# Kernel tuning notes

Measured on AMD Instinct MI355X. Metric: run time of the kernel, lower is better.

## Reference

```python
import jax, jax.numpy as jnp
import numpy as np

N_EXPERTS = 8
D_MODEL = 1024
D_FF = 4096


def setup_inputs() -> dict:
    key = jax.random.key(0)
    k_x, k_idx, k_g, k_u, k_d = jax.random.split(key, 5)
    scale_in = 1.0 / np.sqrt(D_MODEL)
    scale_ff = 1.0 / np.sqrt(D_FF)
    return {
        "x": jax.random.normal(k_x, (2, 1024, D_MODEL), dtype=jnp.float32),
        "expert_idx": jax.random.randint(k_idx, (2, 1024), 0, N_EXPERTS, dtype=jnp.int64),
        "w_gate": jax.random.normal(k_g, (N_EXPERTS, D_MODEL, D_FF), dtype=jnp.float32) * scale_in,
        "w_up": jax.random.normal(k_u, (N_EXPERTS, D_MODEL, D_FF), dtype=jnp.float32) * scale_in,
        "w_down": jax.random.normal(k_d, (N_EXPERTS, D_FF, D_MODEL), dtype=jnp.float32) * scale_ff,
    }


def reference(x, expert_idx, w_gate, w_up, w_down):
    # x: [B, S, D]; expert_idx: [B, S] in [0, N_EXPERTS)
    B, S, D = x.shape
    x_flat = x.reshape(-1, D)                  # [T, D]
    idx_flat = expert_idx.reshape(-1)          # [T]
    out = jnp.zeros_like(x_flat)
    # Faithful per-expert dispatch: each token is processed by exactly one
    # expert's SwiGLU FFN; masked scatter-back combines results.
    for e in range(N_EXPERTS):
        mask = (idx_flat == e)[:, None]        # [T, 1]
        gate = jax.nn.silu(x_flat @ w_gate[e]) # [T, F]
        up = x_flat @ w_up[e]                  # [T, F]
        y = (gate * up) @ w_down[e]            # [T, D]
        out = jnp.where(mask, y, out)
    return out.reshape(B, S, D)
```

## Files before the change

kernel.cpp:

```cpp
#include <hip/hip_runtime.h>
#include <hip/hip_bf16.h>
#include <stdint.h>

#define N_EXPERTS 8
#define D_MODEL   1024
#define D_FF      4096
#define T_TOKENS  2048
#define MT        128
#define MAXT      24
#define KPAD      40

typedef __attribute__((ext_vector_type(8))) short bf16x8;
typedef __attribute__((ext_vector_type(4))) float f32x4;

__device__ __forceinline__ short f2bf(float f) {
    union { float f; uint32_t u; } v; v.f = f;
    uint32_t u = v.u;
    uint32_t r = (u + 0x7fffu + ((u >> 16) & 1u)) >> 16;
    return (short)r;
}

__device__ __forceinline__ uint32_t pack2bf(float a, float b) {
    __hip_bfloat162 h = __float22bfloat162_rn(make_float2(a, b));
    return *(uint32_t*)&h;
}


__global__ void moe_count(const int* __restrict__ idx, int* __restrict__ counts) {
    int t = blockIdx.x * blockDim.x + threadIdx.x;
    if (t < T_TOKENS) atomicAdd(&counts[idx[t]], 1);
}

__global__ void moe_scan(const int* __restrict__ counts, int* __restrict__ offsets,
                         int* __restrict__ ntiles, int* __restrict__ tile_e,
                         int* __restrict__ tile_p0, int* __restrict__ tile_end) {
    if (threadIdx.x == 0 && blockIdx.x == 0) {
        int off = 0, nt = 0;
        for (int e = 0; e < N_EXPERTS; ++e) {
            offsets[e] = off;
            int c = counts[e];
            int end = off + c;
            for (int i = 0; i < c; i += MT) {
                tile_e[nt] = e;
                tile_p0[nt] = off + i;
                tile_end[nt] = end;
                ++nt;
            }
            off = end;
        }
        offsets[N_EXPERTS] = off;
        *ntiles = nt;
    }
}

__global__ void moe_gather(const float* __restrict__ x, const int* __restrict__ idx,
                           const int* __restrict__ offsets, int* __restrict__ cursor,
                           int* __restrict__ tok_of_row, short* __restrict__ Xg) {
    __shared__ int sp;
    int t = blockIdx.x;
    if (threadIdx.x == 0) {
        int e = idx[t];
        int p = offsets[e] + atomicAdd(&cursor[e], 1);
        tok_of_row[p] = t;
        sp = p;
    }
    __syncthreads();
    int p = sp;
    const float4* src = (const float4*)(x + (size_t)t * D_MODEL);
    uint2* dst = (uint2*)(Xg + (size_t)p * D_MODEL);
    int i = threadIdx.x;
    float4 v = src[i];
    uint2 o;
    o.x = pack2bf(v.x, v.y);
    o.y = pack2bf(v.z, v.w);
    dst[i] = o;
}


__launch_bounds__(256)
__global__ void moe_gemm1(const float* __restrict__ wg, const float* __restrict__ wu,
                          const short* __restrict__ Xg, short* __restrict__ h,
                          const int* __restrict__ tile_e, const int* __restrict__ tile_p0,
                          const int* __restrict__ tile_end, const int* __restrict__ ntiles) {
    int ti = blockIdx.y;
    if (ti >= *ntiles) return;
    int e = tile_e[ti], p0 = tile_p0[ti], pend = tile_end[ti];
    int n0 = blockIdx.x * 64;

    __shared__ short Bg[64][KPAD];
    __shared__ short Bu[64][KPAD];

    int tid = threadIdx.x;
    int nl = tid & 63, kc = tid >> 6;
    int lane = tid & 63, w = tid >> 6;
    int col = lane & 15, quad = lane >> 4;

    const float* wgb = wg + (size_t)e * D_MODEL * D_FF + n0 + nl;
    const float* wub = wu + (size_t)e * D_MODEL * D_FF + n0 + nl;

    int row0 = p0 + w * 32 + col;      if (row0 > T_TOKENS - 1) row0 = T_TOKENS - 1;
    int row1 = row0 + 16;              if (row1 > T_TOKENS - 1) row1 = T_TOKENS - 1;
    const short* a0p = Xg + (size_t)row0 * D_MODEL + quad * 8;
    const short* a1p = Xg + (size_t)row1 * D_MODEL + quad * 8;

    f32x4 accg[2][4], accu[2][4];
#pragma unroll
    for (int m = 0; m < 2; ++m)
#pragma unroll
        for (int nf = 0; nf < 4; ++nf) {
            accg[m][nf] = (f32x4){0,0,0,0};
            accu[m][nf] = (f32x4){0,0,0,0};
        }

    for (int k0 = 0; k0 < D_MODEL; k0 += 32) {
        {
            const float* g = wgb + (size_t)(k0 + kc * 8) * D_FF;
            const float* u = wub + (size_t)(k0 + kc * 8) * D_FF;
            float gv[8], uv[8];
#pragma unroll
            for (int j = 0; j < 8; ++j) {
                gv[j] = g[(size_t)j * D_FF];
                uv[j] = u[(size_t)j * D_FF];
            }
            uint4 pg, pu;
            pg.x = pack2bf(gv[0], gv[1]); pg.y = pack2bf(gv[2], gv[3]);
            pg.z = pack2bf(gv[4], gv[5]); pg.w = pack2bf(gv[6], gv[7]);
            pu.x = pack2bf(uv[0], uv[1]); pu.y = pack2bf(uv[2], uv[3]);
            pu.z = pack2bf(uv[4], uv[5]); pu.w = pack2bf(uv[6], uv[7]);
            *(uint4*)&Bg[nl][kc * 8] = pg;
            *(uint4*)&Bu[nl][kc * 8] = pu;
        }
        __syncthreads();
        bf16x8 a0 = *(const bf16x8*)(a0p + k0);
        bf16x8 a1 = *(const bf16x8*)(a1p + k0);
#pragma unroll
        for (int nf = 0; nf < 4; ++nf) {
            bf16x8 bg = *(const bf16x8*)&Bg[nf * 16 + col][quad * 8];
            bf16x8 bu = *(const bf16x8*)&Bu[nf * 16 + col][quad * 8];
            accg[0][nf] = __builtin_amdgcn_mfma_f32_16x16x32_bf16(a0, bg, accg[0][nf], 0, 0, 0);
            accg[1][nf] = __builtin_amdgcn_mfma_f32_16x16x32_bf16(a1, bg, accg[1][nf], 0, 0, 0);
            accu[0][nf] = __builtin_amdgcn_mfma_f32_16x16x32_bf16(a0, bu, accu[0][nf], 0, 0, 0);
            accu[1][nf] = __builtin_amdgcn_mfma_f32_16x16x32_bf16(a1, bu, accu[1][nf], 0, 0, 0);
        }
        __syncthreads();
    }

#pragma unroll
    for (int m = 0; m < 2; ++m) {
#pragma unroll
        for (int r = 0; r < 4; ++r) {
            int mr = p0 + w * 32 + m * 16 + quad * 4 + r;
            if (mr < pend) {
#pragma unroll
                for (int nf = 0; nf < 4; ++nf) {
                    float gv = accg[m][nf][r], uv = accu[m][nf][r];
                    float hv = (gv / (1.f + __expf(-gv))) * uv;
                    h[(size_t)mr * D_FF + n0 + nf * 16 + col] = f2bf(hv);
                }
            }
        }
    }
}


__launch_bounds__(256)
__global__ void moe_gemm2(const float* __restrict__ wd, const short* __restrict__ h,
                          const int* __restrict__ tok_of_row, float* __restrict__ out,
                          const int* __restrict__ tile_e, const int* __restrict__ tile_p0,
                          const int* __restrict__ tile_end, const int* __restrict__ ntiles) {
    int ti = blockIdx.y;
    if (ti >= *ntiles) return;
    int e = tile_e[ti], p0 = tile_p0[ti], pend = tile_end[ti];
    int d0 = blockIdx.x * 64;

    __shared__ short Bd[64][KPAD];

    int tid = threadIdx.x;
    int nl = tid & 63, kc = tid >> 6;
    int lane = tid & 63, w = tid >> 6;
    int col = lane & 15, quad = lane >> 4;

    const float* wb = wd + (size_t)e * D_FF * D_MODEL + d0 + nl;

    int row0 = p0 + w * 32 + col;      if (row0 > T_TOKENS - 1) row0 = T_TOKENS - 1;
    int row1 = row0 + 16;              if (row1 > T_TOKENS - 1) row1 = T_TOKENS - 1;
    const short* a0p = h + (size_t)row0 * D_FF + quad * 8;
    const short* a1p = h + (size_t)row1 * D_FF + quad * 8;

    f32x4 acc[2][4];
#pragma unroll
    for (int m = 0; m < 2; ++m)
#pragma unroll
        for (int nf = 0; nf < 4; ++nf) acc[m][nf] = (f32x4){0,0,0,0};

    for (int k0 = 0; k0 < D_FF; k0 += 32) {
        {
            const float* p = wb + (size_t)(k0 + kc * 8) * D_MODEL;
            float pv[8];
#pragma unroll
            for (int j = 0; j < 8; ++j) pv[j] = p[(size_t)j * D_MODEL];
            uint4 pk;
            pk.x = pack2bf(pv[0], pv[1]); pk.y = pack2bf(pv[2], pv[3]);
            pk.z = pack2bf(pv[4], pv[5]); pk.w = pack2bf(pv[6], pv[7]);
            *(uint4*)&Bd[nl][kc * 8] = pk;
        }
        __syncthreads();
        bf16x8 a0 = *(const bf16x8*)(a0p + k0);
        bf16x8 a1 = *(const bf16x8*)(a1p + k0);
#pragma unroll
        for (int nf = 0; nf < 4; ++nf) {
            bf16x8 b = *(const bf16x8*)&Bd[nf * 16 + col][quad * 8];
            acc[0][nf] = __builtin_amdgcn_mfma_f32_16x16x32_bf16(a0, b, acc[0][nf], 0, 0, 0);
            acc[1][nf] = __builtin_amdgcn_mfma_f32_16x16x32_bf16(a1, b, acc[1][nf], 0, 0, 0);
        }
        __syncthreads();
    }

#pragma unroll
    for (int m = 0; m < 2; ++m) {
#pragma unroll
        for (int r = 0; r < 4; ++r) {
            int mr = p0 + w * 32 + m * 16 + quad * 4 + r;
            if (mr < pend) {
                int t = tok_of_row[mr];
#pragma unroll
                for (int nf = 0; nf < 4; ++nf)
                    out[(size_t)t * D_MODEL + d0 + nf * 16 + col] = acc[m][nf][r];
            }
        }
    }
}


extern "C" void kernel_launch(void* const* d_in, const int* in_sizes, int n_in,
                              void* d_out, int out_size, void* d_ws, size_t ws_size,
                              hipStream_t stream) {
    (void)in_sizes; (void)n_in; (void)out_size; (void)ws_size;
    const float* x   = (const float*)d_in[0];
    const int*   idx = (const int*)d_in[1];
    const float* wg  = (const float*)d_in[2];
    const float* wu  = (const float*)d_in[3];
    const float* wd  = (const float*)d_in[4];
    float* out = (float*)d_out;

    int* ws_i       = (int*)d_ws;
    int* counts     = ws_i;
    int* cursor     = ws_i + 8;
    int* offsets    = ws_i + 16;
    int* ntiles     = ws_i + 25;
    int* tile_e     = ws_i + 32;
    int* tile_p0    = ws_i + 104;
    int* tile_end   = ws_i + 176;
    int* tok_of_row = ws_i + 256;

    short* Xg = (short*)((char*)d_ws + 16384);
    short* h  = (short*)((char*)d_ws + 16384 + (size_t)T_TOKENS * D_MODEL * 2);

    hipMemsetAsync(d_ws, 0, 1024, stream);
    moe_count<<<dim3((T_TOKENS + 255) / 256), 256, 0, stream>>>(idx, counts);
    moe_scan<<<dim3(1), 64, 0, stream>>>(counts, offsets, ntiles, tile_e, tile_p0, tile_end);
    moe_gather<<<dim3(T_TOKENS), 256, 0, stream>>>(x, idx, offsets, cursor, tok_of_row, Xg);
    moe_gemm1<<<dim3(D_FF / 64, MAXT), 256, 0, stream>>>(wg, wu, Xg, h,
                                                         tile_e, tile_p0, tile_end, ntiles);
    moe_gemm2<<<dim3(D_MODEL / 64, MAXT), 256, 0, stream>>>(wd, h, tok_of_row, out,
                                                            tile_e, tile_p0, tile_end, ntiles);
}
```

Baseline: 566.0 us.

## Double-buffer weight tiles, widen K step, shrink gemm2 row tiles, fuse routing

Both GEMM kernels now use double-buffered LDS weight tiles with a K step of 64, so the next tile's global loads are issued before the current tile's MFMAs and one barrier per iteration is removed. gemm2 switches to 64-row tiles with one 16-row fragment per wave, which gives more blocks and better fills the GPU for the down projection. The count and scan kernels are merged into a single routing kernel that builds separate tile lists for each GEMM, dropping a launch. The trade-off is more registers for prefetched data and more LDS use, which may lower occupancy, and the weights in gemm2 are reread more often.

After: 506.7 us. 1.12x faster.

```diff
diff --git a/kernel.cpp b/kernel.cpp
--- a/kernel.cpp
+++ b/kernel.cpp
@@ -6,9 +6,12 @@
 #define D_MODEL   1024
 #define D_FF      4096
 #define T_TOKENS  2048
-#define MT        128
-#define MAXT      24
-#define KPAD      40
+#define MT1       128
+#define MAXT1     24
+#define MT2       64
+#define MAXT2     40
+#define BK        64
+#define KP        72
 
 typedef __attribute__((ext_vector_type(8))) short bf16x8;
 typedef __attribute__((ext_vector_type(4))) float f32x4;
@@ -16,8 +19,7 @@
 __device__ __forceinline__ short f2bf(float f) {
     union { float f; uint32_t u; } v; v.f = f;
     uint32_t u = v.u;
-    uint32_t r = (u + 0x7fffu + ((u >> 16) & 1u)) >> 16;
-    return (short)r;
+    return (short)((u + 0x7fffu + ((u >> 16) & 1u)) >> 16);
 }
 
 __device__ __forceinline__ uint32_t pack2bf(float a, float b) {
@@ -25,31 +27,46 @@
     return *(uint32_t*)&h;
 }
 
-
-__global__ void moe_count(const int* __restrict__ idx, int* __restrict__ counts) {
-    int t = blockIdx.x * blockDim.x + threadIdx.x;
-    if (t < T_TOKENS) atomicAdd(&counts[idx[t]], 1);
-}
-
-__global__ void moe_scan(const int* __restrict__ counts, int* __restrict__ offsets,
-                         int* __restrict__ ntiles, int* __restrict__ tile_e,
-                         int* __restrict__ tile_p0, int* __restrict__ tile_end) {
-    if (threadIdx.x == 0 && blockIdx.x == 0) {
-        int off = 0, nt = 0;
+template<int STRIDE>
+__device__ __forceinline__ void ldw16(float v[16], const float* __restrict__ src) {
+#pragma unroll
+    for (int j = 0; j < 16; ++j) v[j] = src[(size_t)j * STRIDE];
+}
+
+__device__ __forceinline__ void stw16(short* dst, const float v[16]) {
+    uint4 w0, w1;
+    w0.x = pack2bf(v[0], v[1]);  w0.y = pack2bf(v[2], v[3]);
+    w0.z = pack2bf(v[4], v[5]);  w0.w = pack2bf(v[6], v[7]);
+    w1.x = pack2bf(v[8], v[9]);  w1.y = pack2bf(v[10], v[11]);
+    w1.z = pack2bf(v[12], v[13]); w1.w = pack2bf(v[14], v[15]);
+    *(uint4*)dst = w0;
+    *(uint4*)(dst + 8) = w1;
+}
+
+
+__global__ void moe_route(const int* __restrict__ idx, int* __restrict__ offsets,
+                          int* __restrict__ nt1p, int* __restrict__ t1_e,
+                          int* __restrict__ t1_p0, int* __restrict__ t1_end,
+                          int* __restrict__ nt2p, int* __restrict__ t2_e,
+                          int* __restrict__ t2_p0, int* __restrict__ t2_end) {
+    __shared__ int cnt[N_EXPERTS];
+    int tid = threadIdx.x;
+    if (tid < N_EXPERTS) cnt[tid] = 0;
+    __syncthreads();
+    for (int t = tid; t < T_TOKENS; t += 256) atomicAdd(&cnt[idx[t]], 1);
+    __syncthreads();
+    if (tid == 0) {
+        int off = 0, nt1 = 0, nt2 = 0;
         for (int e = 0; e < N_EXPERTS; ++e) {
             offsets[e] = off;
-            int c = counts[e];
-            int end = off + c;
-            for (int i = 0; i < c; i += MT) {
-                tile_e[nt] = e;
-                tile_p0[nt] = off + i;
-                tile_end[nt] = end;
-                ++nt;
-            }
+            int c = cnt[e], end = off + c;
+            for (int i = 0; i < c; i += MT1) { t1_e[nt1] = e; t1_p0[nt1] = off + i; t1_end[nt1] = end; ++nt1; }
+            for (int i = 0; i < c; i += MT2) { t2_e[nt2] = e; t2_p0[nt2] = off + i; t2_end[nt2] = end; ++nt2; }
             off = end;
         }
         offsets[N_EXPERTS] = off;
-        *ntiles = nt;
+        *nt1p = nt1;
+        *nt2p = nt2;
     }
 }
 
@@ -87,16 +104,16 @@
     int e = tile_e[ti], p0 = tile_p0[ti], pend = tile_end[ti];
     int n0 = blockIdx.x * 64;
 
-    __shared__ short Bg[64][KPAD];
-    __shared__ short Bu[64][KPAD];
+    __shared__ short Bg[2][64][KP];
+    __shared__ short Bu[2][64][KP];
 
     int tid = threadIdx.x;
     int nl = tid & 63, kc = tid >> 6;
     int lane = tid & 63, w = tid >> 6;
     int col = lane & 15, quad = lane >> 4;
 
-    const float* wgb = wg + (size_t)e * D_MODEL * D_FF + n0 + nl;
-    const float* wub = wu + (size_t)e * D_MODEL * D_FF + n0 + nl;
+    const float* wgb = wg + (size_t)e * D_MODEL * D_FF + (size_t)(kc * 16) * D_FF + n0 + nl;
+    const float* wub = wu + (size_t)e * D_MODEL * D_FF + (size_t)(kc * 16) * D_FF + n0 + nl;
 
     int row0 = p0 + w * 32 + col;      if (row0 > T_TOKENS - 1) row0 = T_TOKENS - 1;
     int row1 = row0 + 16;              if (row1 > T_TOKENS - 1) row1 = T_TOKENS - 1;
@@ -112,37 +129,54 @@
             accu[m][nf] = (f32x4){0,0,0,0};
         }
 
-    for (int k0 = 0; k0 < D_MODEL; k0 += 32) {
-        {
-            const float* g = wgb + (size_t)(k0 + kc * 8) * D_FF;
-            const float* u = wub + (size_t)(k0 + kc * 8) * D_FF;
-            float gv[8], uv[8];
-#pragma unroll
-            for (int j = 0; j < 8; ++j) {
-                gv[j] = g[(size_t)j * D_FF];
-                uv[j] = u[(size_t)j * D_FF];
-            }
-            uint4 pg, pu;
-            pg.x = pack2bf(gv[0], gv[1]); pg.y = pack2bf(gv[2], gv[3]);
-            pg.z = pack2bf(gv[4], gv[5]); pg.w = pack2bf(gv[6], gv[7]);
-            pu.x = pack2bf(uv[0], uv[1]); pu.y = pack2bf(uv[2], uv[3]);
-            pu.z = pack2bf(uv[4], uv[5]); pu.w = pack2bf(uv[6], uv[7]);
-            *(uint4*)&Bg[nl][kc * 8] = pg;
-            *(uint4*)&Bu[nl][kc * 8] = pu;
-        }
+    {
+        float g0[16], u0[16];
+        ldw16<D_FF>(g0, wgb);
+        ldw16<D_FF>(u0, wub);
+        stw16(&Bg[0][nl][kc * 16], g0);
+        stw16(&Bu[0][nl][kc * 16], u0);
+    }
+    __syncthreads();
+
+    bf16x8 a00 = *(const bf16x8*)(a0p);
+    bf16x8 a01 = *(const bf16x8*)(a0p + 32);
+    bf16x8 a10 = *(const bf16x8*)(a1p);
+    bf16x8 a11 = *(const bf16x8*)(a1p + 32);
+
+    const int NIT = D_MODEL / BK;
+    int p = 0;
+#pragma unroll 1
+    for (int it = 0; it < NIT; ++it) {
+        int kn = (it + 1 == NIT) ? 0 : (it + 1) * BK;
+        float gn[16], un[16];
+        ldw16<D_FF>(gn, wgb + (size_t)kn * D_FF);
+        ldw16<D_FF>(un, wub + (size_t)kn * D_FF);
+        bf16x8 a00n = *(const bf16x8*)(a0p + kn);
+        bf16x8 a01n = *(const bf16x8*)(a0p + kn + 32);
+        bf16x8 a10n = *(const bf16x8*)(a1p + kn);
+        bf16x8 a11n = *(const bf16x8*)(a1p + kn + 32);
+
+#pragma unroll
+        for (int nf = 0; nf < 4; ++nf) {
+            bf16x8 bg0 = *(const bf16x8*)&Bg[p][nf * 16 + col][quad * 8];
+            bf16x8 bg1 = *(const bf16x8*)&Bg[p][nf * 16 + col][32 + quad * 8];
+            bf16x8 bu0 = *(const bf16x8*)&Bu[p][nf * 16 + col][quad * 8];
+            bf16x8 bu1 = *(const bf16x8*)&Bu[p][nf * 16 + col][32 + quad * 8];
+            accg[0][nf] = __builtin_amdgcn_mfma_f32_16x16x32_bf16(a00, bg0, accg[0][nf], 0, 0, 0);
+            accg[0][nf] = __builtin_amdgcn_mfma_f32_16x16x32_bf16(a01, bg1, accg[0][nf], 0, 0, 0);
+            accg[1][nf] = __builtin_amdgcn_mfma_f32_16x16x32_bf16(a10, bg0, accg[1][nf], 0, 0, 0);
+            accg[1][nf] = __builtin_amdgcn_mfma_f32_16x16x32_bf16(a11, bg1, accg[1][nf], 0, 0, 0);
+            accu[0][nf] = __builtin_amdgcn_mfma_f32_16x16x32_bf16(a00, bu0, accu[0][nf], 0, 0, 0);
+            accu[0][nf] = __builtin_amdgcn_mfma_f32_16x16x32_bf16(a01, bu1, accu[0][nf], 0, 0, 0);
+            accu[1][nf] = __builtin_amdgcn_mfma_f32_16x16x32_bf16(a10, bu0, accu[1][nf], 0, 0, 0);
+            accu[1][nf] = __builtin_amdgcn_mfma_f32_16x16x32_bf16(a11, bu1, accu[1][nf], 0, 0, 0);
+        }
+
+        stw16(&Bg[p ^ 1][nl][kc * 16], gn);
+        stw16(&Bu[p ^ 1][nl][kc * 16], un);
+        a00 = a00n; a01 = a01n; a10 = a10n; a11 = a11n;
         __syncthreads();
-        bf16x8 a0 = *(const bf16x8*)(a0p + k0);
-        bf16x8 a1 = *(const bf16x8*)(a1p + k0);
-#pragma unroll
-        for (int nf = 0; nf < 4; ++nf) {
-            bf16x8 bg = *(const bf16x8*)&Bg[nf * 16 + col][quad * 8];
-            bf16x8 bu = *(const bf16x8*)&Bu[nf * 16 + col][quad * 8];
-            accg[0][nf] = __builtin_amdgcn_mfma_f32_16x16x32_bf16(a0, bg, accg[0][nf], 0, 0, 0);
-            accg[1][nf] = __builtin_amdgcn_mfma_f32_16x16x32_bf16(a1, bg, accg[1][nf], 0, 0, 0);
-            accu[0][nf] = __builtin_amdgcn_mfma_f32_16x16x32_bf16(a0, bu, accu[0][nf], 0, 0, 0);
-            accu[1][nf] = __builtin_amdgcn_mfma_f32_16x16x32_bf16(a1, bu, accu[1][nf], 0, 0, 0);
-        }
-        __syncthreads();
+        p ^= 1;
     }
 
 #pragma unroll
@@ -173,60 +207,64 @@
     int e = tile_e[ti], p0 = tile_p0[ti], pend = tile_end[ti];
     int d0 = blockIdx.x * 64;
 
-    __shared__ short Bd[64][KPAD];
+    __shared__ short Bd[2][64][KP];
 
     int tid = threadIdx.x;
     int nl = tid & 63, kc = tid >> 6;
     int lane = tid & 63, w = tid >> 6;
     int col = lane & 15, quad = lane >> 4;
 
-    const float* wb = wd + (size_t)e * D_FF * D_MODEL + d0 + nl;
-
-    int row0 = p0 + w * 32 + col;      if (row0 > T_TOKENS - 1) row0 = T_TOKENS - 1;
-    int row1 = row0 + 16;              if (row1 > T_TOKENS - 1) row1 = T_TOKENS - 1;
+    const float* wb = wd + (size_t)e * D_FF * D_MODEL + (size_t)(kc * 16) * D_MODEL + d0 + nl;
+
+    int row0 = p0 + w * 16 + col;      if (row0 > T_TOKENS - 1) row0 = T_TOKENS - 1;
     const short* a0p = h + (size_t)row0 * D_FF + quad * 8;
-    const short* a1p = h + (size_t)row1 * D_FF + quad * 8;
-
-    f32x4 acc[2][4];
-#pragma unroll
-    for (int m = 0; m < 2; ++m)
-#pragma unroll
-        for (int nf = 0; nf < 4; ++nf) acc[m][nf] = (f32x4){0,0,0,0};
-
-    for (int k0 = 0; k0 < D_FF; k0 += 32) {
-        {
-            const float* p = wb + (size_t)(k0 + kc * 8) * D_MODEL;
-            float pv[8];
-#pragma unroll
-            for (int j = 0; j < 8; ++j) pv[j] = p[(size_t)j * D_MODEL];
-            uint4 pk;
-            pk.x = pack2bf(pv[0], pv[1]); pk.y = pack2bf(pv[2], pv[3]);
-            pk.z = pack2bf(pv[4], pv[5]); pk.w = pack2bf(pv[6], pv[7]);
-            *(uint4*)&Bd[nl][kc * 8] = pk;
-        }
+
+    f32x4 acc[4];
+#pragma unroll
+    for (int nf = 0; nf < 4; ++nf) acc[nf] = (f32x4){0,0,0,0};
+
+    {
+        float w0[16];
+        ldw16<D_MODEL>(w0, wb);
+        stw16(&Bd[0][nl][kc * 16], w0);
+    }
+    __syncthreads();
+
+    bf16x8 a0 = *(const bf16x8*)(a0p);
+    bf16x8 a1 = *(const bf16x8*)(a0p + 32);
+
+    const int NIT = D_FF / BK;
+    int p = 0;
+#pragma unroll 1
+    for (int it = 0; it < NIT; ++it) {
+        int kn = (it + 1 == NIT) ? 0 : (it + 1) * BK;
+        float wn[16];
+        ldw16<D_MODEL>(wn, wb + (size_t)kn * D_MODEL);
+        bf16x8 a0n = *(const bf16x8*)(a0p + kn);
+        bf16x8 a1n = *(const bf16x8*)(a0p + kn + 32);
+
+#pragma unroll
+        for (int nf = 0; nf < 4; ++nf) {
+            bf16x8 b0 = *(const bf16x8*)&Bd[p][nf * 16 + col][quad * 8];
+            bf16x8 b1 = *(const bf16x8*)&Bd[p][nf * 16 + col][32 + quad * 8];
+            acc[nf] = __builtin_amdgcn_mfma_f32_16x16x32_bf16(a0, b0, acc[nf], 0, 0, 0);
+            acc[nf] = __builtin_amdgcn_mfma_f32_16x16x32_bf16(a1, b1, acc[nf], 0, 0, 0);
+        }
+
+        stw16(&Bd[p ^ 1][nl][kc * 16], wn);
+        a0 = a0n; a1 = a1n;
         __syncthreads();
-        bf16x8 a0 = *(const bf16x8*)(a0p + k0);
-        bf16x8 a1 = *(const bf16x8*)(a1p + k0);
-#pragma unroll
-        for (int nf = 0; nf < 4; ++nf) {
-            bf16x8 b = *(const bf16x8*)&Bd[nf * 16 + col][quad * 8];
-            acc[0][nf] = __builtin_amdgcn_mfma_f32_16x16x32_bf16(a0, b, acc[0][nf], 0, 0, 0);
-            acc[1][nf] = __builtin_amdgcn_mfma_f32_16x16x32_bf16(a1, b, acc[1][nf], 0, 0, 0);
-        }
-        __syncthreads();
-    }
-
-#pragma unroll
-    for (int m = 0; m < 2; ++m) {
-#pragma unroll
-        for (int r = 0; r < 4; ++r) {
-            int mr = p0 + w * 32 + m * 16 + quad * 4 + r;
-            if (mr < pend) {
-                int t = tok_of_row[mr];
-#pragma unroll
-                for (int nf = 0; nf < 4; ++nf)
-                    out[(size_t)t * D_MODEL + d0 + nf * 16 + col] = acc[m][nf][r];
-            }
+        p ^= 1;
+    }
+
+#pragma unroll
+    for (int r = 0; r < 4; ++r) {
+        int mr = p0 + w * 16 + quad * 4 + r;
+        if (mr < pend) {
+            int t = tok_of_row[mr];
+#pragma unroll
+            for (int nf = 0; nf < 4; ++nf)
+                out[(size_t)t * D_MODEL + d0 + nf * 16 + col] = acc[nf][r];
         }
     }
 }
@@ -244,24 +282,27 @@
     float* out = (float*)d_out;
 
     int* ws_i       = (int*)d_ws;
-    int* counts     = ws_i;
-    int* cursor     = ws_i + 8;
-    int* offsets    = ws_i + 16;
-    int* ntiles     = ws_i + 25;
-    int* tile_e     = ws_i + 32;
-    int* tile_p0    = ws_i + 104;
-    int* tile_end   = ws_i + 176;
+    int* cursor     = ws_i;
+    int* offsets    = ws_i + 8;
+    int* nt1        = ws_i + 20;
+    int* nt2        = ws_i + 21;
+    int* t1_e       = ws_i + 32;
+    int* t1_p0      = ws_i + 56;
+    int* t1_end     = ws_i + 80;
+    int* t2_e       = ws_i + 104;
+    int* t2_p0      = ws_i + 144;
+    int* t2_end     = ws_i + 184;
     int* tok_of_row = ws_i + 256;
 
     short* Xg = (short*)((char*)d_ws + 16384);
     short* h  = (short*)((char*)d_ws + 16384 + (size_t)T_TOKENS * D_MODEL * 2);
 
-    hipMemsetAsync(d_ws, 0, 1024, stream);
-    moe_count<<<dim3((T_TOKENS + 255) / 256), 256, 0, stream>>>(idx, counts);
-    moe_scan<<<dim3(1), 64, 0, stream>>>(counts, offsets, ntiles, tile_e, tile_p0, tile_end);
+    hipMemsetAsync(d_ws, 0, 128, stream);
+    moe_route<<<dim3(1), 256, 0, stream>>>(idx, offsets, nt1, t1_e, t1_p0, t1_end,
+                                           nt2, t2_e, t2_p0, t2_end);
     moe_gather<<<dim3(T_TOKENS), 256, 0, stream>>>(x, idx, offsets, cursor, tok_of_row, Xg);
-    moe_gemm1<<<dim3(D_FF / 64, MAXT), 256, 0, stream>>>(wg, wu, Xg, h,
-                                                         tile_e, tile_p0, tile_end, ntiles);
-    moe_gemm2<<<dim3(D_MODEL / 64, MAXT), 256, 0, stream>>>(wd, h, tok_of_row, out,
-                                                            tile_e, tile_p0, tile_end, ntiles);
-}
+    moe_gemm1<<<dim3(D_FF / 64, MAXT1), 256, 0, stream>>>(wg, wu, Xg, h,
+                                                          t1_e, t1_p0, t1_end, nt1);
+    moe_gemm2<<<dim3(D_MODEL / 64, MAXT2), 256, 0, stream>>>(wd, h, tok_of_row, out,
+                                                             t2_e, t2_p0, t2_end, nt2);
+}
```
